# Performance work log

Measured on AMD Instinct MI355X. Metric: run time of the kernel, lower is better.

Reference implementation:

```python
import jax, jax.numpy as jnp
import numpy as np
import math

D_MODEL = 512
NUM_HEADS = 8
MAX_LEN = 10000.0


def positional_encoding_2d(seq_len, d_model, H, W, dtype=jnp.float32):
    # position along height repeated across width, and vice versa
    pos_h = jnp.repeat(jnp.arange(H, dtype=dtype), W)  # [H*W]
    pos_w = jnp.tile(jnp.arange(W, dtype=dtype), H)    # [H*W]
    div_term = jnp.exp(jnp.arange(0, d_model, 2, dtype=dtype) * (-(math.log(MAX_LEN) / d_model)))
    div = div_term[: d_model // 4]  # [d_model//4]
    pe = jnp.zeros((seq_len, d_model), dtype=dtype)
    pe = pe.at[:, 0::4].set(jnp.sin(pos_h[:, None] * div))
    pe = pe.at[:, 1::4].set(jnp.cos(pos_h[:, None] * div))
    pe = pe.at[:, 2::4].set(jnp.sin(pos_w[:, None] * div))
    pe = pe.at[:, 3::4].set(jnp.cos(pos_w[:, None] * div))
    return pe


def setup_inputs() -> dict:
    key = jax.random.key(0)
    ks = jax.random.split(key, 6)
    B, C, H, W = 8, D_MODEL, 32, 32
    d = D_MODEL
    s = 1.0 / math.sqrt(d)
    x = jax.random.normal(ks[0], (B, C, H, W), dtype=jnp.float32)
    Wq = jax.random.normal(ks[1], (d, d), dtype=jnp.float32) * s
    Wk = jax.random.normal(ks[2], (d, d), dtype=jnp.float32) * s
    Wv = jax.random.normal(ks[3], (d, d), dtype=jnp.float32) * s
    Wo = jax.random.normal(ks[4], (d, d), dtype=jnp.float32) * s
    bo = jnp.zeros((d,), dtype=jnp.float32)
    gamma = jnp.ones((d,), dtype=jnp.float32)
    beta = jnp.zeros((d,), dtype=jnp.float32)
    return {"x": x, "Wq": Wq, "Wk": Wk, "Wv": Wv, "Wo": Wo, "bo": bo, "gamma": gamma, "beta": beta}


def reference(x, Wq, Wk, Wv, Wo, bo, gamma, beta):
    B, C, H, W = x.shape
    d_model = C
    nh = NUM_HEADS
    dk = d_model // nh
    seq = H * W

    # [B, C, H, W] -> [B, seq, d_model]
    x_seq = x.reshape(B, C, seq).transpose(0, 2, 1)
    pe = positional_encoding_2d(seq, d_model, H, W, dtype=x.dtype)
    x_seq = x_seq + pe[None]
    residual = x_seq

    # QKV projections (torch Linear: y = x @ W.T)
    q = (x_seq @ Wq.T).reshape(B, seq, nh, dk).transpose(0, 2, 1, 3)  # [B, nh, S, dk]
    k = (x_seq @ Wk.T).reshape(B, seq, nh, dk).transpose(0, 2, 1, 3)
    v = (x_seq @ Wv.T).reshape(B, seq, nh, dk).transpose(0, 2, 1, 3)

    scores = jnp.einsum("bhsd,bhtd->bhst", q, k) / math.sqrt(dk)  # [B, nh, S, S]
    weights = jax.nn.softmax(scores, axis=-1)
    # dropout is identity at inference
    attn = jnp.einsum("bhst,bhtd->bhsd", weights, v)  # [B, nh, S, dk]
    attn = attn.transpose(0, 2, 1, 3).reshape(B, seq, d_model)

    out = attn @ Wo.T + bo
    y = out + residual
    mean = jnp.mean(y, axis=-1, keepdims=True)
    var = jnp.var(y, axis=-1, keepdims=True)
    y = (y - mean) / jnp.sqrt(var + 1e-5) * gamma + beta

    return y.transpose(0, 2, 1).reshape(B, C, H, W)
```

## Files before the change

kernel.cpp:

```cpp
#include <hip/hip_runtime.h>
#include <hip/hip_bf16.h>
#include <math.h>

#define DEV static __device__ __forceinline__

typedef unsigned short u16;
typedef unsigned int u32;
typedef __attribute__((ext_vector_type(4))) float f32x4;
typedef __attribute__((ext_vector_type(16))) float f32x16;
typedef __attribute__((ext_vector_type(8))) __bf16 bf16x8;
typedef __attribute__((ext_vector_type(4))) u16 u16x4;
typedef __attribute__((ext_vector_type(4))) u32 u32x4;

DEV u16 f2bf(float f) {
  unsigned u = __float_as_uint(f);
  u += 0x7fffu + ((u >> 16) & 1u);
  return (u16)(u >> 16);
}
DEV float bf2f(u16 x) { return __uint_as_float((u32)x << 16); }

DEV float fexp2(float x) { return __builtin_amdgcn_exp2f(x); }
DEV float fsin_rev(float rev) { return __builtin_amdgcn_sinf(rev); }
DEV float fcos_rev(float rev) { return __builtin_amdgcn_cosf(rev); }

DEV u32 cvt_pk_bf16(float lo, float hi) {
  u32 r;
  asm("v_cvt_pk_bf16_f32 %0, %1, %2" : "=v"(r) : "v"(lo), "v"(hi));
  return r;
}

DEV void perm32swap(u32& a, u32& b) {
  asm("v_permlane32_swap_b32 %0, %1" : "+v"(a), "+v"(b));
}

DEV void gl2lds16(const void* g, void* l) {
  __builtin_amdgcn_global_load_lds(
      (const __attribute__((address_space(1))) void*)g,
      (__attribute__((address_space(3))) void*)l, 16, 0, 0);
}

template<int RPW>
DEV void stage_rows(const u16* __restrict__ g, int gstride, u16* lds, int wave, int lane) {
  const int r_in = lane >> 3, slot = lane & 7;
  const int base_row = wave * RPW;
#pragma unroll
  for (int i = 0; i < RPW / 8; ++i) {
    const int row = base_row + i * 8 + r_in;
    const int sslot = slot ^ (row & 7);
    gl2lds16(g + (size_t)row * gstride + sslot * 8,
             lds + (size_t)(base_row + i * 8) * 64);
  }
}

DEV bf16x8 frag_read(const u16* lds, int row, int kslot) {
  const int slot = kslot ^ (row & 7);
  return *(const bf16x8*)(lds + row * 64 + slot * 8);
}

DEV f32x4 mfma16(bf16x8 a, bf16x8 b, f32x4 c) {
  return __builtin_amdgcn_mfma_f32_16x16x32_bf16(a, b, c, 0, 0, 0);
}
DEV f32x16 mfma32(bf16x8 a, bf16x8 b, f32x16 c) {
  return __builtin_amdgcn_mfma_f32_32x32x16_bf16(a, b, c, 0, 0, 0);
}

__global__ __launch_bounds__(256) void pack_w(
    const float* __restrict__ w0, const float* __restrict__ w1,
    const float* __restrict__ w2, const float* __restrict__ w3,
    u16* __restrict__ dst) {
  const float* src = (blockIdx.y == 0) ? w0 : (blockIdx.y == 1) ? w1
                   : (blockIdx.y == 2) ? w2 : w3;
  const int lane = threadIdx.x & 63, wave = threadIdx.x >> 6;
  const int c16 = blockIdx.x >> 2;
  const int kchunk = (blockIdx.x & 3) * 4 + wave;
  const int cl = lane & 15, ko = lane >> 4;
  const float* s = src + (size_t)(c16 * 16 + cl) * 512 + kchunk * 32 + ko * 8;
  const f32x4 a = *(const f32x4*)(s);
  const f32x4 b = *(const f32x4*)(s + 4);
  u16x4 lo, hi;
#pragma unroll
  for (int j = 0; j < 4; ++j) { lo[j] = f2bf(a[j]); hi[j] = f2bf(b[j]); }
  u16* d = dst + (size_t)blockIdx.y * 262144
               + (size_t)(c16 * 16 + kchunk) * 512 + lane * 8;
  *(u16x4*)(d) = lo;
  *(u16x4*)(d + 4) = hi;
}

__global__ __launch_bounds__(256) void prep_x(
    const float* __restrict__ x, u16* __restrict__ Xp) {
  __shared__ float tile[32][33];
  const int b = blockIdx.z, c0 = blockIdx.y * 32, s0 = blockIdx.x * 32;
  const int t = threadIdx.x;
  const int cf = t >> 5, sf = t & 31;
#pragma unroll
  for (int i = 0; i < 4; ++i) {
    const int c = c0 + cf + i * 8;
    tile[cf + i * 8][sf] = x[((size_t)b * 512 + c) * 1024 + s0 + sf];
  }
  __syncthreads();
  const int cl = t & 31, sl = t >> 5;
  const int cg = c0 + cl;
  const int j = cg >> 2;
  const float dv = fexp2((float)j * -0.051905126482615f);
  const float dv_rev = dv * 0.15915494309189535f;
#pragma unroll
  for (int i = 0; i < 4; ++i) {
    const int s = s0 + sl + i * 8;
    const float pos = (cg & 2) ? (float)(s & 31) : (float)(s >> 5);
    float rev = pos * dv_rev;
    rev = rev - floorf(rev);
    const float pe = (cg & 1) ? fcos_rev(rev) : fsin_rev(rev);
    const float v = tile[cl][sl + i * 8] + pe;
    Xp[((size_t)b * 1024 + s) * 512 + cg] = f2bf(v);
  }
}

__global__ __launch_bounds__(256) void gemm_qkv(
    const u16* __restrict__ Xp, const u16* __restrict__ Wpk,
    u16* __restrict__ Qb, u16* __restrict__ Kb, u16* __restrict__ Vtb,
    float qscale) {
  __shared__ __align__(16) u16 smem[128 * 132];
  u16* As = smem;
  const int t = threadIdx.x, lane = t & 63, wave = t >> 6;
  const int bn0 = blockIdx.x * 128, bm0 = blockIdx.y * 128;
  const int wr = wave >> 1, wc = wave & 1;
  const int colbase = bn0 + wc * 64;
  const int w = colbase >> 9;
  const int cb16 = (colbase & 511) >> 4;
  const u16* Bf = Wpk + (size_t)w * 262144;
  const u16* Ag = Xp + (size_t)bm0 * 512;
  f32x4 acc[4][4] = {};
  for (int kt = 0; kt < 512; kt += 64) {
    __syncthreads();
    stage_rows<32>(Ag + kt, 512, As, wave, lane);
    __syncthreads();
#pragma unroll
    for (int ks = 0; ks < 2; ++ks) {
      const int kc = (kt >> 5) + ks;
      bf16x8 af[4], bfr[4];
#pragma unroll
      for (int n = 0; n < 4; ++n)
        bfr[n] = *(const bf16x8*)(Bf + (size_t)((cb16 + n) * 16 + kc) * 512 + lane * 8);
#pragma unroll
      for (int m = 0; m < 4; ++m)
        af[m] = frag_read(As, wr * 64 + m * 16 + (lane & 15), ks * 4 + (lane >> 4));
#pragma unroll
      for (int m = 0; m < 4; ++m)
#pragma unroll
        for (int n = 0; n < 4; ++n)
          acc[m][n] = mfma16(af[m], bfr[n], acc[m][n]);
    }
  }
  const int cl = lane & 15, rg = (lane >> 4) * 4;
  if (bn0 >= 1024) {
    __syncthreads();
#pragma unroll
    for (int m = 0; m < 4; ++m)
#pragma unroll
      for (int n = 0; n < 4; ++n) {
        const int dvL = wc * 64 + n * 16 + cl;
        const int rowL0 = wr * 64 + m * 16 + rg;
        u16x4 pk;
#pragma unroll
        for (int r = 0; r < 4; ++r) pk[r] = f2bf(acc[m][n][r]);
        *(u16x4*)(smem + dvL * 132 + rowL0) = pk;
      }
    __syncthreads();
    const int dvg0 = bn0 - 1024;
#pragma unroll
    for (int i = 0; i < 16; ++i) {
      const int idx = i * 256 + t;
      const int dv = idx >> 5, ch = (idx & 31) * 4;
      const u16x4 v = *(const u16x4*)(smem + dv * 132 + ch);
      *(u16x4*)(Vtb + (size_t)(dvg0 + dv) * 8192 + bm0 + ch) = v;
    }
  } else {
    u16* dst = (bn0 >= 512) ? Kb : Qb;
    const float al = (bn0 >= 512) ? 1.0f : qscale;
    const int cb = (bn0 & 511) + wc * 64;
#pragma unroll
    for (int m = 0; m < 4; ++m)
#pragma unroll
      for (int n = 0; n < 4; ++n) {
        const int col = cb + n * 16 + cl;
#pragma unroll
        for (int r = 0; r < 4; ++r) {
          const int row = bm0 + wr * 64 + m * 16 + rg + r;
          dst[(size_t)row * 512 + col] = f2bf(acc[m][n][r] * al);
        }
      }
  }
}

__global__ __launch_bounds__(256) void gemm_ln(
    const u16* __restrict__ A, const u16* __restrict__ Wpk,
    const u16* __restrict__ residb, const float* __restrict__ bias,
    const float* __restrict__ gamma, const float* __restrict__ beta,
    float* __restrict__ out) {
  __shared__ __align__(16) u16 smem[34816];
  __shared__ float redsum[4][32], redsq[4][32], srow[32][2];
  const int t = threadIdx.x, lane = t & 63, wave = t >> 6;
  const int m0 = blockIdx.x * 32;
  const int b = m0 >> 10, s0 = m0 & 1023;
  u16* As = smem;
  const u16* Bf = Wpk + (size_t)3 * 262144;
  const u16* Ag = A + (size_t)m0 * 512;
  f32x4 acc[2][8] = {};
  for (int kt = 0; kt < 512; kt += 64) {
    __syncthreads();
    stage_rows<8>(Ag + kt, 512, As, wave, lane);
    __syncthreads();
#pragma unroll
    for (int ks = 0; ks < 2; ++ks) {
      const int kc = (kt >> 5) + ks;
      bf16x8 af[2], bfr[8];
#pragma unroll
      for (int n = 0; n < 8; ++n)
        bfr[n] = *(const bf16x8*)(Bf + (size_t)((wave * 8 + n) * 16 + kc) * 512 + lane * 8);
#pragma unroll
      for (int m = 0; m < 2; ++m)
        af[m] = frag_read(As, m * 16 + (lane & 15), ks * 4 + (lane >> 4));
#pragma unroll
      for (int m = 0; m < 2; ++m)
#pragma unroll
        for (int n = 0; n < 8; ++n)
          acc[m][n] = mfma16(af[m], bfr[n], acc[m][n]);
    }
  }
  __syncthreads();
  float* fsm = (float*)smem;
  float* fw = fsm + wave * (128 * 33);
  const int cl = lane & 15, rg = (lane >> 4) * 4;
  float psum[8], psq[8];
#pragma unroll
  for (int i = 0; i < 8; ++i) { psum[i] = 0.f; psq[i] = 0.f; }
#pragma unroll
  for (int m = 0; m < 2; ++m)
#pragma unroll
    for (int n = 0; n < 8; ++n) {
      const int col_l = n * 16 + cl;
      const int col = wave * 128 + col_l;
      const float bi = bias[col];
#pragma unroll
      for (int r = 0; r < 4; ++r) {
        const int row_l = m * 16 + rg + r;
        const float v = acc[m][n][r] + bi
                      + bf2f(residb[(size_t)(m0 + row_l) * 512 + col]);
        fw[col_l * 33 + row_l] = v;
        psum[m * 4 + r] += v;
        psq[m * 4 + r] += v * v;
      }
    }
#pragma unroll
  for (int i = 0; i < 8; ++i) {
#pragma unroll
    for (int off = 8; off >= 1; off >>= 1) {
      psum[i] += __shfl_xor(psum[i], off);
      psq[i]  += __shfl_xor(psq[i], off);
    }
  }
  if (cl == 0) {
#pragma unroll
    for (int m = 0; m < 2; ++m)
#pragma unroll
      for (int r = 0; r < 4; ++r) {
        const int row_l = m * 16 + rg + r;
        redsum[wave][row_l] = psum[m * 4 + r];
        redsq[wave][row_l]  = psq[m * 4 + r];
      }
  }
  __syncthreads();
  if (t < 32) {
    float s = redsum[0][t] + redsum[1][t] + redsum[2][t] + redsum[3][t];
    float q = redsq[0][t] + redsq[1][t] + redsq[2][t] + redsq[3][t];
    const float mean = s * (1.f / 512.f);
    const float var = q * (1.f / 512.f) - mean * mean;
    srow[t][0] = mean;
    srow[t][1] = rsqrtf(var + 1e-5f);
  }
  __syncthreads();
  const int row = lane & 31, chalf = lane >> 5;
  const float mean = srow[row][0], rstd = srow[row][1];
  float* outb = out + (size_t)b * 512 * 1024 + s0 + row;
#pragma unroll 4
  for (int cc = 0; cc < 64; ++cc) {
    const int col_l = cc * 2 + chalf;
    const int col = wave * 128 + col_l;
    const float v = (fw[col_l * 33 + row] - mean) * rstd;
    outb[(size_t)col * 1024] = v * gamma[col] + beta[col];
  }
}

__global__ __launch_bounds__(256, 2) void attn(
    const u16* __restrict__ Qb, const u16* __restrict__ Kb,
    const u16* __restrict__ Vt, u16* __restrict__ Ob) {
  __shared__ __align__(16) u16 Ks[2][64 * 64];
  __shared__ __align__(16) u16 Vs[2][64 * 64];
  const int t = threadIdx.x, lane = t & 63, wave = t >> 6;
  const int wg = blockIdx.x;
  const int b = wg & 7, h = (wg >> 3) & 7, qt = wg >> 6;
  const int qsub = wave & 1, half = wave >> 1;
  const int ql = lane & 31, hl = lane >> 5;
  const int q0 = qt * 64 + qsub * 32;
  bf16x8 bq[4];
  {
    const u16* qrow = Qb + ((size_t)b * 1024 + q0 + ql) * 512 + h * 64 + hl * 8;
#pragma unroll
    for (int c = 0; c < 4; ++c) bq[c] = *(const bf16x8*)(qrow + c * 16);
  }
  f32x16 ot[2] = {};
  float m_run = -1e30f, l_run = 0.f;
  u16* stg_dst = qsub ? Vs[half] : Ks[half];
  for (int i = 0; i < 8; ++i) {
    const int kb = half * 512 + i * 64;
    {
      const int r_in = lane >> 3, slot = lane & 7;
      const u16* src; size_t gs;
      if (qsub) { src = Vt + (size_t)(h * 64) * 8192 + (size_t)b * 1024 + kb; gs = 8192; }
      else      { src = Kb + ((size_t)b * 1024 + kb) * 512 + h * 64;          gs = 512; }
#pragma unroll
      for (int j = 0; j < 8; ++j) {
        const int row = j * 8 + r_in;
        const int ss = slot ^ (row & 7);
        gl2lds16(src + (size_t)row * gs + ss * 8, stg_dst + j * 512);
      }
    }
    __syncthreads();
    f32x16 st[2] = {};
    __builtin_amdgcn_s_setprio(1);
#pragma unroll
    for (int c = 0; c < 4; ++c) {
      bf16x8 a0 = frag_read(Ks[half], ql, c * 2 + hl);
      bf16x8 a1 = frag_read(Ks[half], 32 + ql, c * 2 + hl);
      st[0] = mfma32(a0, bq[c], st[0]);
      st[1] = mfma32(a1, bq[c], st[1]);
    }
    __builtin_amdgcn_s_setprio(0);
    float m0[8];
#pragma unroll
    for (int i2 = 0; i2 < 8; ++i2)
      m0[i2] = fmaxf(fmaxf(st[0][i2], st[0][i2 + 8]), fmaxf(st[1][i2], st[1][i2 + 8]));
#pragma unroll
    for (int i2 = 0; i2 < 4; ++i2) m0[i2] = fmaxf(m0[i2], m0[i2 + 4]);
    float mx = fmaxf(fmaxf(m0[0], m0[1]), fmaxf(m0[2], m0[3]));
    mx = fmaxf(mx, __shfl_xor(mx, 32));
    if (!__all(mx <= m_run + 8.f)) {
      const float mn = fmaxf(m_run, mx);
      const float sc = fexp2(m_run - mn);
      m_run = mn;
      l_run *= sc;
      ot[0] *= sc;
      ot[1] *= sc;
    }
#pragma unroll
    for (int i2 = 0; i2 < 16; ++i2) {
      st[0][i2] = fexp2(st[0][i2] - m_run);
      st[1][i2] = fexp2(st[1][i2] - m_run);
    }
    float s0[8];
#pragma unroll
    for (int i2 = 0; i2 < 8; ++i2)
      s0[i2] = (st[0][i2] + st[0][i2 + 8]) + (st[1][i2] + st[1][i2 + 8]);
#pragma unroll
    for (int i2 = 0; i2 < 4; ++i2) s0[i2] = s0[i2] + s0[i2 + 4];
    float rs = (s0[0] + s0[1]) + (s0[2] + s0[3]);
    rs += __shfl_xor(rs, 32);
    l_run += rs;
    __builtin_amdgcn_s_setprio(1);
#pragma unroll
    for (int c = 0; c < 4; ++c) {
      const int kf = c >> 1, i0 = (c & 1) * 4;
      u32 w0 = cvt_pk_bf16(st[kf][2 * i0 + 0], st[kf][2 * i0 + 1]);
      u32 w1 = cvt_pk_bf16(st[kf][2 * i0 + 2], st[kf][2 * i0 + 3]);
      u32 w2 = cvt_pk_bf16(st[kf][2 * i0 + 4], st[kf][2 * i0 + 5]);
      u32 w3 = cvt_pk_bf16(st[kf][2 * i0 + 6], st[kf][2 * i0 + 7]);
      perm32swap(w0, w2);
      perm32swap(w1, w3);
      u32x4 wv; wv.x = w0; wv.y = w1; wv.z = w2; wv.w = w3;
      bf16x8 bp = *(bf16x8*)&wv;
      bf16x8 v0 = frag_read(Vs[half], ql, c * 2 + hl);
      bf16x8 v1 = frag_read(Vs[half], 32 + ql, c * 2 + hl);
      ot[0] = mfma32(v0, bp, ot[0]);
      ot[1] = mfma32(v1, bp, ot[1]);
    }
    __builtin_amdgcn_s_setprio(0);
    __syncthreads();
  }
  float* Om = (float*)&Ks[0][0] + qsub * 2048;
  float* Ml = (float*)&Vs[0][0];
  if (wave >= 2) {
#pragma unroll
    for (int df = 0; df < 2; ++df)
#pragma unroll
      for (int r = 0; r < 16; ++r) {
        const int dr = (r & 3) + 8 * (r >> 2) + 4 * hl;
        Om[(df * 32 + dr) * 32 + ql] = ot[df][r];
      }
    if (hl == 0) {
      Ml[qsub * 64 + ql] = m_run;
      Ml[qsub * 64 + 32 + ql] = l_run;
    }
    __syncthreads();
  } else {
    __syncthreads();
    const float m2 = Ml[qsub * 64 + ql];
    const float l2 = Ml[qsub * 64 + 32 + ql];
    const float m = fmaxf(m_run, m2);
    const float a = fexp2(m_run - m);
    const float bsc = fexp2(m2 - m);
    const float inv = 1.f / (l_run * a + l2 * bsc);
    u16* orow = Ob + ((size_t)b * 1024 + q0 + ql) * 512 + h * 64;
#pragma unroll
    for (int df = 0; df < 2; ++df)
#pragma unroll
      for (int r = 0; r < 16; ++r) {
        const int dr = (r & 3) + 8 * (r >> 2) + 4 * hl;
        const float v = ot[df][r] * a + Om[(df * 32 + dr) * 32 + ql] * bsc;
        orow[df * 32 + dr] = f2bf(v * inv);
      }
  }
}

extern "C" void kernel_launch(void* const* d_in, const int* in_sizes, int n_in,
                              void* d_out, int out_size, void* d_ws, size_t ws_size,
                              hipStream_t stream) {
  const float* x     = (const float*)d_in[0];
  const float* Wq    = (const float*)d_in[1];
  const float* Wk    = (const float*)d_in[2];
  const float* Wv    = (const float*)d_in[3];
  const float* Wo    = (const float*)d_in[4];
  const float* bo    = (const float*)d_in[5];
  const float* gamma = (const float*)d_in[6];
  const float* beta  = (const float*)d_in[7];
  char* ws = (char*)d_ws;
  const size_t MB = 1048576;
  u16*   Xp    = (u16*)(ws);
  u16*   Wpk   = (u16*)(ws + 8 * MB);
  u16*   Qb    = (u16*)(ws + 10 * MB);
  u16*   Kb    = (u16*)(ws + 18 * MB);
  u16*   Vtb   = (u16*)(ws + 26 * MB);
  u16*   Ob    = (u16*)(ws + 34 * MB);

  pack_w<<<dim3(128, 4), 256, 0, stream>>>(Wq, Wk, Wv, Wo, Wpk);
  prep_x<<<dim3(32, 16, 8), 256, 0, stream>>>(x, Xp);
  gemm_qkv<<<dim3(12, 64), 256, 0, stream>>>(Xp, Wpk, Qb, Kb, Vtb,
                                             0.125f * 1.44269504088896f);
  attn<<<1024, 256, 0, stream>>>(Qb, Kb, Vtb, Ob);
  gemm_ln<<<256, 256, 0, stream>>>(Ob, Wpk, Xp, bo, gamma, beta,
                                   (float*)d_out);
}
```

Baseline: 95.58 us.

## Store activations in MFMA fragment layout and drop LDS staging in GEMMs

Producer kernels (prep_x and attn epilogue) now write X and attention output directly in the packed MFMA fragment layout used for weights, so gemm_qkv and gemm_ln load A fragments straight from global memory without LDS staging or barriers. This removes shared-memory staging and syncthreads from the GEMM K loops. The costs are scattered 2-byte stores in prep_x, the gathered residual reads in gemm_ln, and A fragments being reloaded from global/L2 by each wave instead of shared through LDS.

```diff
diff --git a/kernel.cpp b/kernel.cpp
--- a/kernel.cpp
+++ b/kernel.cpp
@@ -62,6 +62,11 @@
 }
 DEV f32x16 mfma32(bf16x8 a, bf16x8 b, f32x16 c) {
   return __builtin_amdgcn_mfma_f32_32x32x16_bf16(a, b, c, 0, 0, 0);
+}
+
+DEV size_t frag_elem(int row, int col) {
+  return ((size_t)((row >> 4) * 16 + (col >> 5))) * 512
+       + ((row & 15) + 16 * ((col >> 3) & 3)) * 8 + (col & 7);
 }
 
 __global__ __launch_bounds__(256) void pack_w(
@@ -87,7 +92,7 @@
 }
 
 __global__ __launch_bounds__(256) void prep_x(
-    const float* __restrict__ x, u16* __restrict__ Xp) {
+    const float* __restrict__ x, u16* __restrict__ Xa) {
   __shared__ float tile[32][33];
   const int b = blockIdx.z, c0 = blockIdx.y * 32, s0 = blockIdx.x * 32;
   const int t = threadIdx.x;
@@ -111,16 +116,16 @@
     rev = rev - floorf(rev);
     const float pe = (cg & 1) ? fcos_rev(rev) : fsin_rev(rev);
     const float v = tile[cl][sl + i * 8] + pe;
-    Xp[((size_t)b * 1024 + s) * 512 + cg] = f2bf(v);
+    const int row = b * 1024 + s;
+    Xa[frag_elem(row, cg)] = f2bf(v);
   }
 }
 
 __global__ __launch_bounds__(256) void gemm_qkv(
-    const u16* __restrict__ Xp, const u16* __restrict__ Wpk,
+    const u16* __restrict__ Xa, const u16* __restrict__ Wpk,
     u16* __restrict__ Qb, u16* __restrict__ Kb, u16* __restrict__ Vtb,
     float qscale) {
   __shared__ __align__(16) u16 smem[128 * 132];
-  u16* As = smem;
   const int t = threadIdx.x, lane = t & 63, wave = t >> 6;
   const int bn0 = blockIdx.x * 128, bm0 = blockIdx.y * 128;
   const int wr = wave >> 1, wc = wave & 1;
@@ -128,32 +133,25 @@
   const int w = colbase >> 9;
   const int cb16 = (colbase & 511) >> 4;
   const u16* Bf = Wpk + (size_t)w * 262144;
-  const u16* Ag = Xp + (size_t)bm0 * 512;
+  const int row16base = (bm0 >> 4) + wr * 4;
   f32x4 acc[4][4] = {};
-  for (int kt = 0; kt < 512; kt += 64) {
-    __syncthreads();
-    stage_rows<32>(Ag + kt, 512, As, wave, lane);
-    __syncthreads();
-#pragma unroll
-    for (int ks = 0; ks < 2; ++ks) {
-      const int kc = (kt >> 5) + ks;
-      bf16x8 af[4], bfr[4];
+#pragma unroll 4
+  for (int kc = 0; kc < 16; ++kc) {
+    bf16x8 af[4], bfr[4];
+#pragma unroll
+    for (int n = 0; n < 4; ++n)
+      bfr[n] = *(const bf16x8*)(Bf + (size_t)((cb16 + n) * 16 + kc) * 512 + lane * 8);
+#pragma unroll
+    for (int m = 0; m < 4; ++m)
+      af[m] = *(const bf16x8*)(Xa + (size_t)((row16base + m) * 16 + kc) * 512 + lane * 8);
+#pragma unroll
+    for (int m = 0; m < 4; ++m)
 #pragma unroll
       for (int n = 0; n < 4; ++n)
-        bfr[n] = *(const bf16x8*)(Bf + (size_t)((cb16 + n) * 16 + kc) * 512 + lane * 8);
-#pragma unroll
-      for (int m = 0; m < 4; ++m)
-        af[m] = frag_read(As, wr * 64 + m * 16 + (lane & 15), ks * 4 + (lane >> 4));
-#pragma unroll
-      for (int m = 0; m < 4; ++m)
-#pragma unroll
-        for (int n = 0; n < 4; ++n)
-          acc[m][n] = mfma16(af[m], bfr[n], acc[m][n]);
-    }
+        acc[m][n] = mfma16(af[m], bfr[n], acc[m][n]);
   }
   const int cl = lane & 15, rg = (lane >> 4) * 4;
   if (bn0 >= 1024) {
-    __syncthreads();
 #pragma unroll
     for (int m = 0; m < 4; ++m)
 #pragma unroll
@@ -193,42 +191,33 @@
 }
 
 __global__ __launch_bounds__(256) void gemm_ln(
-    const u16* __restrict__ A, const u16* __restrict__ Wpk,
-    const u16* __restrict__ residb, const float* __restrict__ bias,
+    const u16* __restrict__ Obf, const u16* __restrict__ Wpk,
+    const u16* __restrict__ Xa, const float* __restrict__ bias,
     const float* __restrict__ gamma, const float* __restrict__ beta,
     float* __restrict__ out) {
-  __shared__ __align__(16) u16 smem[34816];
+  __shared__ float fsm[4 * 128 * 33];
   __shared__ float redsum[4][32], redsq[4][32], srow[32][2];
   const int t = threadIdx.x, lane = t & 63, wave = t >> 6;
   const int m0 = blockIdx.x * 32;
   const int b = m0 >> 10, s0 = m0 & 1023;
-  u16* As = smem;
+  const int row16 = m0 >> 4;
   const u16* Bf = Wpk + (size_t)3 * 262144;
-  const u16* Ag = A + (size_t)m0 * 512;
   f32x4 acc[2][8] = {};
-  for (int kt = 0; kt < 512; kt += 64) {
-    __syncthreads();
-    stage_rows<8>(Ag + kt, 512, As, wave, lane);
-    __syncthreads();
-#pragma unroll
-    for (int ks = 0; ks < 2; ++ks) {
-      const int kc = (kt >> 5) + ks;
-      bf16x8 af[2], bfr[8];
+#pragma unroll 4
+  for (int kc = 0; kc < 16; ++kc) {
+    bf16x8 af[2], bfr[8];
+#pragma unroll
+    for (int n = 0; n < 8; ++n)
+      bfr[n] = *(const bf16x8*)(Bf + (size_t)((wave * 8 + n) * 16 + kc) * 512 + lane * 8);
+#pragma unroll
+    for (int m = 0; m < 2; ++m)
+      af[m] = *(const bf16x8*)(Obf + (size_t)((row16 + m) * 16 + kc) * 512 + lane * 8);
+#pragma unroll
+    for (int m = 0; m < 2; ++m)
 #pragma unroll
       for (int n = 0; n < 8; ++n)
-        bfr[n] = *(const bf16x8*)(Bf + (size_t)((wave * 8 + n) * 16 + kc) * 512 + lane * 8);
-#pragma unroll
-      for (int m = 0; m < 2; ++m)
-        af[m] = frag_read(As, m * 16 + (lane & 15), ks * 4 + (lane >> 4));
-#pragma unroll
-      for (int m = 0; m < 2; ++m)
-#pragma unroll
-        for (int n = 0; n < 8; ++n)
-          acc[m][n] = mfma16(af[m], bfr[n], acc[m][n]);
-    }
-  }
-  __syncthreads();
-  float* fsm = (float*)smem;
+        acc[m][n] = mfma16(af[m], bfr[n], acc[m][n]);
+  }
   float* fw = fsm + wave * (128 * 33);
   const int cl = lane & 15, rg = (lane >> 4) * 4;
   float psum[8], psq[8];
@@ -245,7 +234,7 @@
       for (int r = 0; r < 4; ++r) {
         const int row_l = m * 16 + rg + r;
         const float v = acc[m][n][r] + bi
-                      + bf2f(residb[(size_t)(m0 + row_l) * 512 + col]);
+                      + bf2f(Xa[frag_elem(m0 + row_l, col)]);
         fw[col_l * 33 + row_l] = v;
         psum[m * 4 + r] += v;
         psq[m * 4 + r] += v * v;
@@ -293,7 +282,7 @@
 
 __global__ __launch_bounds__(256, 2) void attn(
     const u16* __restrict__ Qb, const u16* __restrict__ Kb,
-    const u16* __restrict__ Vt, u16* __restrict__ Ob) {
+    const u16* __restrict__ Vt, u16* __restrict__ Obf) {
   __shared__ __align__(16) u16 Ks[2][64 * 64];
   __shared__ __align__(16) u16 Vs[2][64 * 64];
   const int t = threadIdx.x, lane = t & 63, wave = t >> 6;
@@ -409,15 +398,33 @@
     const float a = fexp2(m_run - m);
     const float bsc = fexp2(m2 - m);
     const float inv = 1.f / (l_run * a + l2 * bsc);
-    u16* orow = Ob + ((size_t)b * 1024 + q0 + ql) * 512 + h * 64;
+    float v[2][16];
 #pragma unroll
     for (int df = 0; df < 2; ++df)
 #pragma unroll
       for (int r = 0; r < 16; ++r) {
         const int dr = (r & 3) + 8 * (r >> 2) + 4 * hl;
-        const float v = ot[df][r] * a + Om[(df * 32 + dr) * 32 + ql] * bsc;
-        orow[df * 32 + dr] = f2bf(v * inv);
-      }
+        v[df][r] = (ot[df][r] * a + Om[(df * 32 + dr) * 32 + ql] * bsc) * inv;
+      }
+    const int q = b * 1024 + q0 + ql;
+#pragma unroll
+    for (int p = 0; p < 4; ++p) {
+      const int jjA = 2 * p, jjB = 2 * p + 1;
+      const int dfA = jjA >> 2, rA = (jjA & 3) * 4;
+      const int dfB = jjB >> 2, rB = (jjB & 3) * 4;
+      u32 a0 = cvt_pk_bf16(v[dfA][rA + 0], v[dfA][rA + 1]);
+      u32 a1 = cvt_pk_bf16(v[dfA][rA + 2], v[dfA][rA + 3]);
+      u32 b0 = cvt_pk_bf16(v[dfB][rB + 0], v[dfB][rB + 1]);
+      u32 b1 = cvt_pk_bf16(v[dfB][rB + 2], v[dfB][rB + 3]);
+      perm32swap(a0, b0);
+      perm32swap(a1, b1);
+      const int jj = 2 * p + hl;
+      const int d0 = h * 64 + jj * 8;
+      u32x4 wv; wv.x = a0; wv.y = a1; wv.z = b0; wv.w = b1;
+      u16* dst = Obf + ((size_t)((q >> 4) * 16 + (d0 >> 5))) * 512
+                     + ((q & 15) + 16 * ((d0 >> 3) & 3)) * 8;
+      *(u32x4*)dst = wv;
+    }
   }
 }
 
@@ -434,18 +441,18 @@
   const float* beta  = (const float*)d_in[7];
   char* ws = (char*)d_ws;
   const size_t MB = 1048576;
-  u16*   Xp    = (u16*)(ws);
+  u16*   Xa    = (u16*)(ws);
   u16*   Wpk   = (u16*)(ws + 8 * MB);
   u16*   Qb    = (u16*)(ws + 10 * MB);
   u16*   Kb    = (u16*)(ws + 18 * MB);
   u16*   Vtb   = (u16*)(ws + 26 * MB);
-  u16*   Ob    = (u16*)(ws + 34 * MB);
+  u16*   Obf   = (u16*)(ws + 34 * MB);
 
   pack_w<<<dim3(128, 4), 256, 0, stream>>>(Wq, Wk, Wv, Wo, Wpk);
-  prep_x<<<dim3(32, 16, 8), 256, 0, stream>>>(x, Xp);
-  gemm_qkv<<<dim3(12, 64), 256, 0, stream>>>(Xp, Wpk, Qb, Kb, Vtb,
+  prep_x<<<dim3(32, 16, 8), 256, 0, stream>>>(x, Xa);
+  gemm_qkv<<<dim3(12, 64), 256, 0, stream>>>(Xa, Wpk, Qb, Kb, Vtb,
                                              0.125f * 1.44269504088896f);
-  attn<<<1024, 256, 0, stream>>>(Qb, Kb, Vtb, Ob);
-  gemm_ln<<<256, 256, 0, stream>>>(Ob, Wpk, Xp, bo, gamma, beta,
+  attn<<<1024, 256, 0, stream>>>(Qb, Kb, Vtb, Obf);
+  gemm_ln<<<256, 256, 0, stream>>>(Obf, Wpk, Xa, bo, gamma, beta,
                                    (float*)d_out);
 }
```

Result: no change. 95.95 us (+0.4%).
